# Kernel tuning notes

Measured on AMD Instinct MI355X. Metric: run time of the kernel, lower is better.

The kernel has to match this reference:

```python
import math
import jax, jax.numpy as jnp
import numpy as np

NUM_BUCKETS = 32
MAX_DISTANCE = 128
N_HEADS = 16
D_KV = 64


def _relative_position_bucket(relative_position, num_buckets=NUM_BUCKETS, max_distance=MAX_DISTANCE):
    # bidirectional (encoder) version, faithful to T5Attention._relative_position_bucket
    nb = num_buckets // 2
    rel_buckets = (relative_position > 0).astype(jnp.int32) * nb
    rp = jnp.abs(relative_position)
    max_exact = nb // 2
    is_small = rp < max_exact
    # log-spaced buckets for large distances; clamp arg of log to >=1 to avoid -inf
    rp_large = max_exact + (
        jnp.log(jnp.maximum(rp, 1).astype(jnp.float32) / max_exact)
        / math.log(max_distance / max_exact)
        * (nb - max_exact)
    ).astype(jnp.int32)
    rp_large = jnp.minimum(rp_large, nb - 1)
    return rel_buckets + jnp.where(is_small, rp, rp_large)


def setup_inputs() -> dict:
    key = jax.random.key(0)
    ks = jax.random.split(key, 6)
    B, S, D = 2, 2048, 1024
    scale = 0.02
    return {
        "hidden_states": jax.random.normal(ks[0], (B, S, D), dtype=jnp.float32),
        "Wq": jax.random.normal(ks[1], (D, N_HEADS * D_KV), dtype=jnp.float32) * scale,
        "Wk": jax.random.normal(ks[2], (D, N_HEADS * D_KV), dtype=jnp.float32) * scale,
        "Wv": jax.random.normal(ks[3], (D, N_HEADS * D_KV), dtype=jnp.float32) * scale,
        "Wo": jax.random.normal(ks[4], (N_HEADS * D_KV, D), dtype=jnp.float32) * scale,
        "rel_bias": jax.random.normal(ks[5], (NUM_BUCKETS, N_HEADS), dtype=jnp.float32),
    }


def reference(hidden_states, Wq, Wk, Wv, Wo, rel_bias):
    B, S, D = hidden_states.shape
    H, dk = N_HEADS, D_KV
    q = (hidden_states @ Wq).reshape(B, S, H, dk)
    k = (hidden_states @ Wk).reshape(B, S, H, dk)
    v = (hidden_states @ Wv).reshape(B, S, H, dk)

    pos = jnp.arange(S)
    relative_position = pos[None, :] - pos[:, None]          # [S_q, S_k]
    buckets = _relative_position_bucket(relative_position)    # [S_q, S_k]
    bias = rel_bias[buckets].transpose(2, 0, 1)               # [H, S_q, S_k]

    # T5 attention: NO 1/sqrt(d) scaling
    scores = jnp.einsum('bqhd,bkhd->bhqk', q, k) + bias[None]
    attn = jax.nn.softmax(scores, axis=-1)
    ctx = jnp.einsum('bhqk,bkhd->bqhd', attn, v).reshape(B, S, H * dk)
    return ctx @ Wo
```

## Files before the change

kernel.cpp:

```cpp
#include <hip/hip_runtime.h>
#include <hip/hip_bf16.h>
#include <stdint.h>

#define S_LEN 2048
#define NH 16
#define NB_DELTA (2*S_LEN-1)
#define LOG2E 1.4426950408889634f

typedef __attribute__((ext_vector_type(8))) __bf16 bf16x8;
typedef __attribute__((ext_vector_type(4))) float f32x4;

__device__ __forceinline__ unsigned short f2bf(float f){
    union { float f; unsigned int u; } v; v.f = f;
    unsigned int u = v.u;
    return (unsigned short)((u + 0x7FFFu + ((u >> 16) & 1u)) >> 16);
}
__device__ __forceinline__ float bf2f(unsigned short u){
    union { unsigned int u; float f; } v; v.u = ((unsigned int)u) << 16;
    return v.f;
}
__device__ __forceinline__ unsigned int pkbf(float a, float b){
    __hip_bfloat162 h = __float22bfloat162_rn(float2{a, b});
    unsigned int u;
    __builtin_memcpy(&u, &h, 4);
    return u;
}
#if __has_builtin(__builtin_amdgcn_exp2f)
__device__ __forceinline__ float fexp2(float x){ return __builtin_amdgcn_exp2f(x); }
#else
__device__ __forceinline__ float fexp2(float x){ return __expf(x * 0.69314718056f); }
#endif

__device__ __forceinline__ void gload16(const void* g, void* l){
    __builtin_amdgcn_global_load_lds(
        (const __attribute__((address_space(1))) void*)(uintptr_t)g,
        (__attribute__((address_space(3))) void*)(uintptr_t)l, 16, 0, 0);
}

__global__ __launch_bounds__(256) void prep_kernel(
    const float* __restrict__ hs, unsigned short* __restrict__ hsb,
    const float* __restrict__ W0, const float* __restrict__ W1,
    const float* __restrict__ W2, const float* __restrict__ W3,
    unsigned short* __restrict__ D0, unsigned short* __restrict__ D1,
    unsigned short* __restrict__ D2, unsigned short* __restrict__ D3,
    const float* __restrict__ rel_bias, float* __restrict__ biasT){
    if (blockIdx.z == 4) {
        int bi = blockIdx.y * 32 + blockIdx.x;
        for (int it = 0; it < 4; it++) {
            int i = bi * 4096 + it * 1024 + threadIdx.x * 4;
            float4 f = *(const float4*)(hs + i);
            ushort4 o;
            o.x = f2bf(f.x); o.y = f2bf(f.y); o.z = f2bf(f.z); o.w = f2bf(f.w);
            *(ushort4*)(hsb + i) = o;
        }
        if (bi < 16) {
            int t = bi * 256 + threadIdx.x;
            if (t < NB_DELTA) {
                int delta = t - (S_LEN - 1);
                int bucket = (delta > 0) ? 16 : 0;
                int a = delta < 0 ? -delta : delta;
                int b;
                if (a < 8) b = a;
                else {
                    int bl = 33 - __builtin_clz(a * a);
                    b = bl < 15 ? bl : 15;
                }
                bucket += b;
                for (int h = 0; h < NH; h++)
                    biasT[h * NB_DELTA + t] = (rel_bias[bucket * NH + h] - 16.f) * LOG2E;
            }
        }
        return;
    }
    const float* src; unsigned short* dst;
    switch (blockIdx.z) {
        case 0: src = W0; dst = D0; break;
        case 1: src = W1; dst = D1; break;
        case 2: src = W2; dst = D2; break;
        default: src = W3; dst = D3; break;
    }
    __shared__ float tile[32][33];
    int bx = blockIdx.x, by = blockIdx.y;
    int tx = threadIdx.x & 31, ty = threadIdx.x >> 5;
    for (int i = 0; i < 4; i++)
        tile[ty + 8*i][tx] = src[(size_t)(by*32 + ty + 8*i) * 1024 + bx*32 + tx];
    __syncthreads();
    for (int i = 0; i < 4; i++)
        dst[(size_t)(bx*32 + ty + 8*i) * 1024 + by*32 + tx] = f2bf(tile[tx][ty + 8*i]);
}

template<int MODE, int BM>
__global__ __launch_bounds__(256) void gemm_bt_kernel(const unsigned short* __restrict__ A,
                                                      const unsigned short* __restrict__ BT,
                                                      float* __restrict__ C0,
                                                      unsigned short* __restrict__ C1,
                                                      unsigned short* __restrict__ Vt,
                                                      int Kdim, int ldc){
    constexpr int IT = BM / 32;
    __shared__ __align__(16) unsigned short As[BM * 64];
    __shared__ __align__(16) unsigned short Bs[128 * 64];
    const int t = threadIdx.x;
    const int wave = t >> 6, lane = t & 63;
    const int quad = lane >> 4, l16 = lane & 15;
    const int wm = (wave >> 1) * (BM / 2), wn = (wave & 1) * 64;
    const size_t row0 = (size_t)blockIdx.y * BM, col0 = (size_t)blockIdx.x * 128;

    const int srow8 = lane >> 3;
    const int gg = (lane & 7) ^ srow8;
    const unsigned short* gA = A  + (row0 + wave * 8 + srow8) * (size_t)Kdim + gg * 8;
    const unsigned short* gB = BT + (col0 + wave * 8 + srow8) * (size_t)Kdim + gg * 8;

    f32x4 acc[IT][4] = {};

    for (int kt = 0; kt < Kdim; kt += 64) {
        for (int p = 0; p < BM / 32; p++)
            gload16(gA + (size_t)(p * 32) * Kdim + kt, &As[(p * 32 + wave * 8) * 64]);
        for (int p = 0; p < 4; p++)
            gload16(gB + (size_t)(p * 32) * Kdim + kt, &Bs[(p * 32 + wave * 8) * 64]);
        __syncthreads();
        bf16x8 a[2][IT], b[2][4];
        for (int ks = 0; ks < 2; ks++) {
            for (int i = 0; i < IT; i++)
                a[ks][i] = *(const bf16x8*)(&As[(wm + i*16 + l16) * 64 + (((ks*4 + quad) ^ (l16 & 7)) * 8)]);
            for (int j = 0; j < 4; j++)
                b[ks][j] = *(const bf16x8*)(&Bs[(wn + j*16 + l16) * 64 + (((ks*4 + quad) ^ (l16 & 7)) * 8)]);
        }
        for (int ks = 0; ks < 2; ks++)
            for (int i = 0; i < IT; i++)
                for (int j = 0; j < 4; j++)
                    acc[i][j] = __builtin_amdgcn_mfma_f32_16x16x32_bf16(a[ks][i], b[ks][j], acc[i][j], 0, 0, 0);
        __syncthreads();
    }
    for (int i = 0; i < IT; i++)
        for (int j = 0; j < 4; j++) {
            size_t r0 = row0 + wm + i*16 + quad*4;
            size_t c  = col0 + wn + j*16 + l16;
            if (MODE == 0) {
                for (int r = 0; r < 4; r++)
                    C0[(r0 + r) * ldc + c] = acc[i][j][r];
            } else if (c < 2048) {
                float qs = (c < 1024) ? LOG2E : 1.0f;
                for (int r = 0; r < 4; r++)
                    C1[(r0 + r) * ldc + c] = f2bf(acc[i][j][r] * qs);
            } else {
                size_t bb = r0 >> 11, s = r0 & 2047;
                ushort4 o;
                o.x = f2bf(acc[i][j][0]); o.y = f2bf(acc[i][j][1]);
                o.z = f2bf(acc[i][j][2]); o.w = f2bf(acc[i][j][3]);
                *(ushort4*)(Vt + ((bb << 10) + (c - 2048)) * 2048 + s) = o;
            }
        }
}

__global__ __launch_bounds__(512, 4) void flash16_kernel(
    const unsigned short* __restrict__ qkb,
    const unsigned short* __restrict__ vt,
    const float* __restrict__ biasT,
    unsigned short* __restrict__ ctxpb,
    float* __restrict__ rsbuf)
{
    const int lin  = blockIdx.x;
    const int logi = (lin & 7) * 128 + (lin >> 3);
    const int qt = logi & 7, h = (logi >> 3) & 15;
    const int zz = logi >> 7;
    const int b = zz >> 2, ck = zz & 3;
    const int kt0 = ck << 9;
    const int t = threadIdx.x;
    const int w = t >> 6, lane = t & 63, quad = lane >> 4, l16 = lane & 15;
    const int q0 = qt * 256;

    __shared__ __align__(16) unsigned short Ks[2][64 * 64];
    __shared__ __align__(16) unsigned short Vs[2][64 * 64];
    __shared__ float bias_b[768];

    {
        const float* bsrc = biasT + h * NB_DELTA + (kt0 - q0 + 1792);
        for (int u = t; u < 767; u += 512) bias_b[u] = bsrc[u];
    }
    const int srow8 = lane >> 3;
    const int gg = (lane & 7) ^ srow8;
    const int swz = (l16 & 7) * 8;
    const unsigned short* kbase = qkb + (size_t)(b * S_LEN + w * 8 + srow8) * 2048 + 1024 + h * 64 + gg * 8;
    const unsigned short* vbase = vt + (size_t)(b * 1024 + h * 64 + w * 8 + srow8) * 2048 + gg * 8;
    gload16(kbase + (size_t)kt0 * 2048, &Ks[0][(w * 8) * 64]);
    gload16(vbase + kt0,                &Vs[0][(w * 8) * 64]);

    bf16x8 qb[2][2];
    {
        const unsigned short* qbase =
            qkb + (size_t)(b * S_LEN + q0 + w * 32 + l16) * 2048 + h * 64 + quad * 8;
        for (int nt = 0; nt < 2; nt++)
            for (int ks = 0; ks < 2; ks++)
                qb[ks][nt] = *(const bf16x8*)(qbase + (size_t)nt * 16 * 2048 + ks * 32);
    }
    __syncthreads();

    bf16x8 onesA = {};
    if (l16 == 0) {
        const __bf16 one = (__bf16)1.0f;
        for (int e = 0; e < 8; e++) onesA[e] = one;
    }

    f32x4 ctx[4][2] = {};
    f32x4 rsacc[2] = {};
    const int ib0 = 255 + quad * 4 - w * 32 - l16;

    int cur = 0;
    for (int i = 0; i < 8; i++) {
        if (i < 7) {
            int ktn = kt0 + (i + 1) * 64;
            gload16(kbase + (size_t)ktn * 2048, &Ks[cur ^ 1][(w * 8) * 64]);
            gload16(vbase + ktn,                &Vs[cur ^ 1][(w * 8) * 64]);
        }
        f32x4 st[4][2];
        const int ibt = ib0 + i * 64;
        for (int nt = 0; nt < 2; nt++)
            for (int nb = 0; nb < 4; nb++) {
                const float* bp = &bias_b[ibt - nt * 16 + nb * 16];
                st[nb][nt][0] = bp[0]; st[nb][nt][1] = bp[1];
                st[nb][nt][2] = bp[2]; st[nb][nt][3] = bp[3];
            }
        __builtin_amdgcn_s_setprio(1);
        for (int ks = 0; ks < 2; ks++)
            for (int nb = 0; nb < 4; nb++) {
                bf16x8 ka = *(const bf16x8*)&Ks[cur][(nb * 16 + l16) * 64 + (((ks * 4 + quad) * 8) ^ swz)];
                st[nb][0] = __builtin_amdgcn_mfma_f32_16x16x32_bf16(ka, qb[ks][0], st[nb][0], 0, 0, 0);
                st[nb][1] = __builtin_amdgcn_mfma_f32_16x16x32_bf16(ka, qb[ks][1], st[nb][1], 0, 0, 0);
            }
        __builtin_amdgcn_s_setprio(0);
        uint2 pk[2][4];
        for (int nt = 0; nt < 2; nt++)
            for (int nb = 0; nb < 4; nb++) {
                float e0 = fexp2(st[nb][nt][0]);
                float e1 = fexp2(st[nb][nt][1]);
                float e2 = fexp2(st[nb][nt][2]);
                float e3 = fexp2(st[nb][nt][3]);
                pk[nt][nb].x = pkbf(e0, e1);
                pk[nt][nb].y = pkbf(e2, e3);
            }
        __builtin_amdgcn_s_setprio(1);
        for (int ks = 0; ks < 2; ks++) {
            bf16x8 pbf[2];
            for (int nt = 0; nt < 2; nt++) {
                uint2 x0 = pk[nt][2 * ks], x1 = pk[nt][2 * ks + 1];
                auto sA = __builtin_amdgcn_permlane32_swap(x0.x, x1.x, false, false);
                auto sB = __builtin_amdgcn_permlane16_swap(sA[0], sA[1], false, false);
                auto sC = __builtin_amdgcn_permlane32_swap(x0.y, x1.y, false, false);
                auto sD = __builtin_amdgcn_permlane16_swap(sC[0], sC[1], false, false);
                unsigned int u4[4] = {sB[0], sD[0], sB[1], sD[1]};
                __builtin_memcpy(&pbf[nt], u4, 16);
            }
            rsacc[0] = __builtin_amdgcn_mfma_f32_16x16x32_bf16(onesA, pbf[0], rsacc[0], 0, 0, 0);
            rsacc[1] = __builtin_amdgcn_mfma_f32_16x16x32_bf16(onesA, pbf[1], rsacc[1], 0, 0, 0);
            for (int nd = 0; nd < 4; nd++) {
                bf16x8 va = *(const bf16x8*)&Vs[cur][(nd * 16 + l16) * 64 + (((ks * 4 + quad) * 8) ^ swz)];
                ctx[nd][0] = __builtin_amdgcn_mfma_f32_16x16x32_bf16(va, pbf[0], ctx[nd][0], 0, 0, 0);
                ctx[nd][1] = __builtin_amdgcn_mfma_f32_16x16x32_bf16(va, pbf[1], ctx[nd][1], 0, 0, 0);
            }
        }
        __builtin_amdgcn_s_setprio(0);
        __syncthreads();
        cur ^= 1;
    }
    unsigned short* cp = ctxpb + (size_t)ck * 4096 * 1024;
    for (int nt = 0; nt < 2; nt++) {
        int row = b * S_LEN + q0 + w * 32 + nt * 16 + l16;
        if (quad == 0) rsbuf[((size_t)ck * 4096 + row) * 16 + h] = rsacc[nt][0];
        for (int nd = 0; nd < 4; nd++) {
            uint2 pk2;
            pk2.x = pkbf(ctx[nd][nt][0], ctx[nd][nt][1]);
            pk2.y = pkbf(ctx[nd][nt][2], ctx[nd][nt][3]);
            *(uint2*)&cp[(size_t)row * 1024 + h * 64 + nd * 16 + quad * 4] = pk2;
        }
    }
}

__global__ __launch_bounds__(256) void combine_kernel(const unsigned short* __restrict__ ctxpb,
                                                      const float* __restrict__ rsbuf,
                                                      unsigned short* __restrict__ ctxb){
    int e = blockIdx.x * 256 + threadIdx.x;
    int row = e >> 8;
    int c4 = (e & 255) * 4;
    int h = c4 >> 6;
    float l = 0.f;
    for (int p = 0; p < 4; p++) l += rsbuf[((size_t)p * 4096 + row) * 16 + h];
    float s0 = 0.f, s1 = 0.f, s2 = 0.f, s3 = 0.f;
    for (int p = 0; p < 4; p++) {
        ushort4 a = *(const ushort4*)&ctxpb[(size_t)p * 4096 * 1024 + (size_t)row * 1024 + c4];
        s0 += bf2f(a.x); s1 += bf2f(a.y); s2 += bf2f(a.z); s3 += bf2f(a.w);
    }
    float inv = 1.f / l;
    uint2 o;
    o.x = pkbf(s0 * inv, s1 * inv);
    o.y = pkbf(s2 * inv, s3 * inv);
    *(uint2*)&ctxb[(size_t)row * 1024 + c4] = o;
}

extern "C" void kernel_launch(void* const* d_in, const int* in_sizes, int n_in,
                              void* d_out, int out_size, void* d_ws, size_t ws_size,
                              hipStream_t stream) {
    const float* hs       = (const float*)d_in[0];
    const float* Wq       = (const float*)d_in[1];
    const float* Wk       = (const float*)d_in[2];
    const float* Wv       = (const float*)d_in[3];
    const float* Wo       = (const float*)d_in[4];
    const float* rel_bias = (const float*)d_in[5];
    float* out = (float*)d_out;

    char* ws = (char*)d_ws;
    float* biasT          = (float*)ws;           ws += 262144;
    unsigned short* hsb   = (unsigned short*)ws;  ws += 8388608;
    unsigned short* WT    = (unsigned short*)ws;  ws += 6291456;
    unsigned short* WoT   = (unsigned short*)ws;  ws += 2097152;
    unsigned short* qkb   = (unsigned short*)ws;  ws += 16777216;
    unsigned short* Vtg   = (unsigned short*)ws;  ws += 8388608;
    unsigned short* ctxpb = (unsigned short*)ws;  ws += 33554432;
    float* rsbuf          = (float*)ws;
    unsigned short* ctxb  = hsb;

    prep_kernel<<<dim3(32, 32, 5), 256, 0, stream>>>(
        hs, hsb, Wq, Wk, Wv, Wo,
        WT, WT + 1024 * 1024, WT + 2 * 1024 * 1024, WoT, rel_bias, biasT);

    gemm_bt_kernel<1, 64><<<dim3(24, 64), 256, 0, stream>>>(hsb, WT, nullptr, qkb, Vtg, 1024, 2048);
    flash16_kernel<<<dim3(1024), 512, 0, stream>>>(qkb, Vtg, biasT, ctxpb, rsbuf);
    combine_kernel<<<4096, 256, 0, stream>>>(ctxpb, rsbuf, ctxb);
    gemm_bt_kernel<0, 64><<<dim3(8, 64), 256, 0, stream>>>(ctxb, WoT, out, nullptr, nullptr, 1024, 1024);
}
```

Baseline: 194.5 us.

## Halve flash split-K chunks and fuse partial combine into output GEMM

The attention kernel now splits the key dimension into 2 chunks instead of 4. Each block loops over 1024 keys with a larger bias window, and the grid drops to 512 blocks. The separate combine kernel is removed. The output projection GEMM gains a mode that loads both partial context tiles and the row sums into registers, normalises them, and writes bf16 into shared memory, prefetching the next K-step. This removes a kernel launch and the write and re-read of a combined context buffer. In exchange, the flash grid has less parallelism, and the GEMM's A operand goes through registers instead of direct global-to-LDS loads.

```diff
diff --git a/kernel.cpp b/kernel.cpp
--- a/kernel.cpp
+++ b/kernel.cpp
@@ -95,6 +95,7 @@
                                                       float* __restrict__ C0,
                                                       unsigned short* __restrict__ C1,
                                                       unsigned short* __restrict__ Vt,
+                                                      const float* __restrict__ RS,
                                                       int Kdim, int ldc){
     constexpr int IT = BM / 32;
     __shared__ __align__(16) unsigned short As[BM * 64];
@@ -112,11 +113,43 @@
 
     f32x4 acc[IT][4] = {};
 
+    bf16x8 pa0[2], pa1[2];
+    float ra[2], rb[2];
+    auto issueA2 = [&](int kt){
+        for (int p = 0; p < 2; p++) {
+            size_t row = row0 + p * 32 + wave * 8 + srow8;
+            const unsigned short* pp = A + row * 1024 + kt + gg * 8;
+            pa0[p] = *(const bf16x8*)pp;
+            pa1[p] = *(const bf16x8*)(pp + (size_t)4096 * 1024);
+            int head = kt >> 6;
+            ra[p] = RS[row * 16 + head];
+            rb[p] = RS[(4096 + row) * 16 + head];
+        }
+    };
+    if (MODE == 2) issueA2(0);
+
     for (int kt = 0; kt < Kdim; kt += 64) {
-        for (int p = 0; p < BM / 32; p++)
-            gload16(gA + (size_t)(p * 32) * Kdim + kt, &As[(p * 32 + wave * 8) * 64]);
+        if (MODE == 2) {
+            for (int p = 0; p < 2; p++) {
+                float inv = 1.f / (ra[p] + rb[p]);
+                unsigned int u4[4];
+                for (int e = 0; e < 4; e++) {
+                    float x0 = (float)pa0[p][2 * e]     + (float)pa1[p][2 * e];
+                    float x1 = (float)pa0[p][2 * e + 1] + (float)pa1[p][2 * e + 1];
+                    u4[e] = pkbf(x0 * inv, x1 * inv);
+                }
+                bf16x8 pv;
+                __builtin_memcpy(&pv, u4, 16);
+                *(bf16x8*)&As[(p * 32 + wave * 8) * 64 + lane * 8] = pv;
+            }
+        } else {
+            for (int p = 0; p < BM / 32; p++)
+                gload16(gA + (size_t)(p * 32) * Kdim + kt, &As[(p * 32 + wave * 8) * 64]);
+        }
         for (int p = 0; p < 4; p++)
             gload16(gB + (size_t)(p * 32) * Kdim + kt, &Bs[(p * 32 + wave * 8) * 64]);
+        if (MODE == 2 && kt + 64 < Kdim)
+            issueA2(kt + 64);
         __syncthreads();
         bf16x8 a[2][IT], b[2][4];
         for (int ks = 0; ks < 2; ks++) {
@@ -135,7 +168,7 @@
         for (int j = 0; j < 4; j++) {
             size_t r0 = row0 + wm + i*16 + quad*4;
             size_t c  = col0 + wn + j*16 + l16;
-            if (MODE == 0) {
+            if (MODE == 0 || MODE == 2) {
                 for (int r = 0; r < 4; r++)
                     C0[(r0 + r) * ldc + c] = acc[i][j][r];
             } else if (c < 2048) {
@@ -152,7 +185,7 @@
         }
 }
 
-__global__ __launch_bounds__(512, 4) void flash16_kernel(
+__global__ __launch_bounds__(512, 4) void flash17_kernel(
     const unsigned short* __restrict__ qkb,
     const unsigned short* __restrict__ vt,
     const float* __restrict__ biasT,
@@ -160,22 +193,22 @@
     float* __restrict__ rsbuf)
 {
     const int lin  = blockIdx.x;
-    const int logi = (lin & 7) * 128 + (lin >> 3);
+    const int logi = (lin & 7) * 64 + (lin >> 3);
     const int qt = logi & 7, h = (logi >> 3) & 15;
     const int zz = logi >> 7;
-    const int b = zz >> 2, ck = zz & 3;
-    const int kt0 = ck << 9;
+    const int b = zz >> 1, ck = zz & 1;
+    const int kt0 = ck << 10;
     const int t = threadIdx.x;
     const int w = t >> 6, lane = t & 63, quad = lane >> 4, l16 = lane & 15;
     const int q0 = qt * 256;
 
     __shared__ __align__(16) unsigned short Ks[2][64 * 64];
     __shared__ __align__(16) unsigned short Vs[2][64 * 64];
-    __shared__ float bias_b[768];
+    __shared__ float bias_b[1280];
 
     {
         const float* bsrc = biasT + h * NB_DELTA + (kt0 - q0 + 1792);
-        for (int u = t; u < 767; u += 512) bias_b[u] = bsrc[u];
+        for (int u = t; u < 1279; u += 512) bias_b[u] = bsrc[u];
     }
     const int srow8 = lane >> 3;
     const int gg = (lane & 7) ^ srow8;
@@ -206,8 +239,8 @@
     const int ib0 = 255 + quad * 4 - w * 32 - l16;
 
     int cur = 0;
-    for (int i = 0; i < 8; i++) {
-        if (i < 7) {
+    for (int i = 0; i < 16; i++) {
+        if (i < 15) {
             int ktn = kt0 + (i + 1) * 64;
             gload16(kbase + (size_t)ktn * 2048, &Ks[cur ^ 1][(w * 8) * 64]);
             gload16(vbase + ktn,                &Vs[cur ^ 1][(w * 8) * 64]);
@@ -275,27 +308,6 @@
     }
 }
 
-__global__ __launch_bounds__(256) void combine_kernel(const unsigned short* __restrict__ ctxpb,
-                                                      const float* __restrict__ rsbuf,
-                                                      unsigned short* __restrict__ ctxb){
-    int e = blockIdx.x * 256 + threadIdx.x;
-    int row = e >> 8;
-    int c4 = (e & 255) * 4;
-    int h = c4 >> 6;
-    float l = 0.f;
-    for (int p = 0; p < 4; p++) l += rsbuf[((size_t)p * 4096 + row) * 16 + h];
-    float s0 = 0.f, s1 = 0.f, s2 = 0.f, s3 = 0.f;
-    for (int p = 0; p < 4; p++) {
-        ushort4 a = *(const ushort4*)&ctxpb[(size_t)p * 4096 * 1024 + (size_t)row * 1024 + c4];
-        s0 += bf2f(a.x); s1 += bf2f(a.y); s2 += bf2f(a.z); s3 += bf2f(a.w);
-    }
-    float inv = 1.f / l;
-    uint2 o;
-    o.x = pkbf(s0 * inv, s1 * inv);
-    o.y = pkbf(s2 * inv, s3 * inv);
-    *(uint2*)&ctxb[(size_t)row * 1024 + c4] = o;
-}
-
 extern "C" void kernel_launch(void* const* d_in, const int* in_sizes, int n_in,
                               void* d_out, int out_size, void* d_ws, size_t ws_size,
                               hipStream_t stream) {
@@ -314,16 +326,14 @@
     unsigned short* WoT   = (unsigned short*)ws;  ws += 2097152;
     unsigned short* qkb   = (unsigned short*)ws;  ws += 16777216;
     unsigned short* Vtg   = (unsigned short*)ws;  ws += 8388608;
-    unsigned short* ctxpb = (unsigned short*)ws;  ws += 33554432;
+    unsigned short* ctxpb = (unsigned short*)ws;  ws += 16777216;
     float* rsbuf          = (float*)ws;
-    unsigned short* ctxb  = hsb;
 
     prep_kernel<<<dim3(32, 32, 5), 256, 0, stream>>>(
         hs, hsb, Wq, Wk, Wv, Wo,
         WT, WT + 1024 * 1024, WT + 2 * 1024 * 1024, WoT, rel_bias, biasT);
 
-    gemm_bt_kernel<1, 64><<<dim3(24, 64), 256, 0, stream>>>(hsb, WT, nullptr, qkb, Vtg, 1024, 2048);
-    flash16_kernel<<<dim3(1024), 512, 0, stream>>>(qkb, Vtg, biasT, ctxpb, rsbuf);
-    combine_kernel<<<4096, 256, 0, stream>>>(ctxpb, rsbuf, ctxb);
-    gemm_bt_kernel<0, 64><<<dim3(8, 64), 256, 0, stream>>>(ctxb, WoT, out, nullptr, nullptr, 1024, 1024);
-}
+    gemm_bt_kernel<1, 64><<<dim3(24, 64), 256, 0, stream>>>(hsb, WT, nullptr, qkb, Vtg, nullptr, 1024, 2048);
+    flash17_kernel<<<dim3(512), 512, 0, stream>>>(qkb, Vtg, biasT, ctxpb, rsbuf);
+    gemm_bt_kernel<2, 64><<<dim3(8, 64), 256, 0, stream>>>(ctxpb, WoT, out, nullptr, nullptr, rsbuf, 1024, 1024);
+}
```

Measured after the change: 190.7 us. No clear change (-2.0%).
